# Performance work log

Hardware: AMD Instinct MI355X
Metric: run time of the kernel (lower is better)

The kernel has to match this reference:

```python
import jax, jax.numpy as jnp
import numpy as np

N_TOKENS = 16384
HIDDEN = 2048
N_EXPERTS = 256
N_GROUPS = 8
TOPK_GROUPS = 4
TOPK = 8
ROUTE_SCALE = 2.5


def setup_inputs() -> dict:
    key = jax.random.key(0)
    k1, k2, k3 = jax.random.split(key, 3)
    x = jax.random.normal(k1, (N_TOKENS, HIDDEN), dtype=jnp.float32)
    weight = jax.random.normal(k2, (N_EXPERTS, HIDDEN), dtype=jnp.float32) * 0.02
    bias = jax.random.normal(k3, (N_EXPERTS,), dtype=jnp.float32) * 0.02
    return {"x": x, "weight": weight, "bias": bias}


def reference(x, weight, bias):
    # linear scoring: [N, E]
    scores = jnp.einsum("nd,ed->ne", x, weight) + bias
    scores = jax.nn.sigmoid(scores)  # score_func == 'sigmoid'
    original_scores = scores
    # bias is not None -> add bias to routing scores
    scores = scores + bias
    n = x.shape[0]
    # grouped routing: [N, G, E/G]
    scores_g = scores.reshape(n, N_GROUPS, N_EXPERTS // N_GROUPS)
    # bias present -> group score = sum of top-2 per group
    top2_vals, _ = jax.lax.top_k(scores_g, 2)
    group_scores = top2_vals.sum(axis=-1)  # [N, G]
    _, grp_idx = jax.lax.top_k(group_scores, TOPK_GROUPS)  # [N, topk_groups]
    keep = jnp.zeros((n, N_GROUPS), dtype=bool).at[
        jnp.arange(n)[:, None], grp_idx
    ].set(True)
    masked = jnp.where(keep[:, :, None], scores_g, -jnp.inf).reshape(n, N_EXPERTS)
    # final top-k experts over masked scores
    _, indices = jax.lax.top_k(masked, TOPK)  # [N, topk]
    weights = jnp.take_along_axis(original_scores, indices, axis=1)
    # sigmoid -> normalize selected weights
    weights = weights / weights.sum(axis=-1, keepdims=True)
    weights = (weights * ROUTE_SCALE).astype(x.dtype)
    return weights, indices
```

## Files before the change

### kernel.cpp

```cpp
#include <hip/hip_runtime.h>
#include <math.h>

#define NT 16384
#define HID 2048
#define NE 256
#define NG 8
#define TOPG 4
#define TOPKK 8

constexpr int BM = 64;
constexpr int KC = 32;

__global__ __launch_bounds__(512) void score_kernel(
    const float* __restrict__ x, const float* __restrict__ w,
    const float* __restrict__ bias, double* __restrict__ sd)
{
    __shared__ float xs[KC][BM];
    __shared__ float wsm[KC][NE];

    const int tid = threadIdx.x;
    const int tx = tid & 31;
    const int ty = tid >> 5;
    const int m0 = blockIdx.x * BM;

    const int xrow = tid & 63;
    const int xko  = (tid >> 6) * 4;
    const int wexp = tid & 255;
    const int wko  = (tid >> 8) * 16;

    double accd[4][8];
#pragma unroll
    for (int mi = 0; mi < 4; mi++)
#pragma unroll
        for (int j = 0; j < 8; j++) accd[mi][j] = 0.0;

    const float* wbase = w + (size_t)wexp * HID + wko;
    const float* xbase = x + (size_t)(m0 + xrow) * HID + xko;

    for (int k0 = 0; k0 < HID; k0 += KC) {
        float4 wv0 = *(const float4*)(wbase + k0 + 0);
        float4 wv1 = *(const float4*)(wbase + k0 + 4);
        float4 wv2 = *(const float4*)(wbase + k0 + 8);
        float4 wv3 = *(const float4*)(wbase + k0 + 12);
        float4 xv  = *(const float4*)(xbase + k0);

        __syncthreads();

        wsm[wko +  0][wexp] = wv0.x; wsm[wko +  1][wexp] = wv0.y;
        wsm[wko +  2][wexp] = wv0.z; wsm[wko +  3][wexp] = wv0.w;
        wsm[wko +  4][wexp] = wv1.x; wsm[wko +  5][wexp] = wv1.y;
        wsm[wko +  6][wexp] = wv1.z; wsm[wko +  7][wexp] = wv1.w;
        wsm[wko +  8][wexp] = wv2.x; wsm[wko +  9][wexp] = wv2.y;
        wsm[wko + 10][wexp] = wv2.z; wsm[wko + 11][wexp] = wv2.w;
        wsm[wko + 12][wexp] = wv3.x; wsm[wko + 13][wexp] = wv3.y;
        wsm[wko + 14][wexp] = wv3.z; wsm[wko + 15][wexp] = wv3.w;
        xs[xko + 0][xrow] = xv.x;
        xs[xko + 1][xrow] = xv.y;
        xs[xko + 2][xrow] = xv.z;
        xs[xko + 3][xrow] = xv.w;

        __syncthreads();

        float accf[4][8];

        {
            float4 a  = *(const float4*)&xs[0][ty * 4];
            float4 b0 = *(const float4*)&wsm[0][tx * 4];
            float4 b1 = *(const float4*)&wsm[0][128 + tx * 4];
            float av[4] = {a.x, a.y, a.z, a.w};
            float bv[8] = {b0.x, b0.y, b0.z, b0.w, b1.x, b1.y, b1.z, b1.w};
#pragma unroll
            for (int mi = 0; mi < 4; mi++)
#pragma unroll
                for (int j = 0; j < 8; j++)
                    accf[mi][j] = av[mi] * bv[j];
        }

#pragma unroll
        for (int kk = 1; kk < KC; kk++) {
            float4 a  = *(const float4*)&xs[kk][ty * 4];
            float4 b0 = *(const float4*)&wsm[kk][tx * 4];
            float4 b1 = *(const float4*)&wsm[kk][128 + tx * 4];
            float av[4] = {a.x, a.y, a.z, a.w};
            float bv[8] = {b0.x, b0.y, b0.z, b0.w, b1.x, b1.y, b1.z, b1.w};
#pragma unroll
            for (int mi = 0; mi < 4; mi++)
#pragma unroll
                for (int j = 0; j < 8; j++)
                    accf[mi][j] = fmaf(av[mi], bv[j], accf[mi][j]);
        }

#pragma unroll
        for (int mi = 0; mi < 4; mi++)
#pragma unroll
            for (int j = 0; j < 8; j++) accd[mi][j] += (double)accf[mi][j];
    }

#pragma unroll
    for (int mi = 0; mi < 4; mi++) {
        const size_t row = (size_t)(m0 + ty * 4 + mi) * NE;
#pragma unroll
        for (int j = 0; j < 8; j++) {
            const int n = (j < 4) ? (tx * 4 + j) : (128 + tx * 4 + (j - 4));
            double z = accd[mi][j] + (double)bias[n];
            double s = 1.0 / (1.0 + exp(-z));
            sd[row + n] = s;
        }
    }
}

__global__ __launch_bounds__(256) void route_kernel(
    const double* __restrict__ sd, const float* __restrict__ bias,
    float* __restrict__ wout, float* __restrict__ iout)
{
    const int lane = threadIdx.x & 63;
    const int wid  = threadIdx.x >> 6;
    const int tok  = blockIdx.x * 4 + wid;
    const double* srow = sd + (size_t)tok * NE;
    const int e0 = lane * 4;

    const double NEG = -__builtin_inf();

    double s0 = srow[e0 + 0], s1 = srow[e0 + 1], s2 = srow[e0 + 2], s3 = srow[e0 + 3];
    double sb0 = s0 + (double)bias[e0 + 0];
    double sb1 = s1 + (double)bias[e0 + 1];
    double sb2 = s2 + (double)bias[e0 + 2];
    double sb3 = s3 + (double)bias[e0 + 3];

    double m1 = sb0, m2 = NEG;
    if (sb1 > m1) { m2 = m1; m1 = sb1; } else if (sb1 > m2) m2 = sb1;
    if (sb2 > m1) { m2 = m1; m1 = sb2; } else if (sb2 > m2) m2 = sb2;
    if (sb3 > m1) { m2 = m1; m1 = sb3; } else if (sb3 > m2) m2 = sb3;

#pragma unroll
    for (int mask = 1; mask <= 4; mask <<= 1) {
        double o1 = __shfl_xor(m1, mask);
        double o2 = __shfl_xor(m2, mask);
        double n1 = fmax(m1, o1);
        double n2 = fmax(fmin(m1, o1), fmax(m2, o2));
        m1 = n1; m2 = n2;
    }
    double gs = m1 + m2;

    double g[8];
#pragma unroll
    for (int j = 0; j < 8; j++) g[j] = __shfl(gs, j * 8);

    const int myg = lane >> 3;
    int rank = 0;
#pragma unroll
    for (int j = 0; j < 8; j++)
        rank += (g[j] > g[myg] || (g[j] == g[myg] && j < myg)) ? 1 : 0;
    const bool keep = (rank < TOPG);

    double v0 = keep ? sb0 : NEG;
    double v1 = keep ? sb1 : NEG;
    double v2 = keep ? sb2 : NEG;
    double v3 = keep ? sb3 : NEG;

    double wv[TOPKK];
    int    idx[TOPKK];

#pragma unroll
    for (int r = 0; r < TOPKK; r++) {
        double bvv = v0; int bi = e0;
        if (v1 > bvv) { bvv = v1; bi = e0 + 1; }
        if (v2 > bvv) { bvv = v2; bi = e0 + 2; }
        if (v3 > bvv) { bvv = v3; bi = e0 + 3; }
#pragma unroll
        for (int mask = 1; mask <= 32; mask <<= 1) {
            double ov = __shfl_xor(bvv, mask);
            int    oi = __shfl_xor(bi, mask);
            if (ov > bvv || (ov == bvv && oi < bi)) { bvv = ov; bi = oi; }
        }
        const int sel   = bi & 3;
        const int owner = bi >> 2;
        double cands = (sel == 0) ? s0 : (sel == 1) ? s1 : (sel == 2) ? s2 : s3;
        wv[r]  = __shfl(cands, owner);
        idx[r] = bi;
        if (lane == owner) {
            if (sel == 0) v0 = NEG;
            else if (sel == 1) v1 = NEG;
            else if (sel == 2) v2 = NEG;
            else v3 = NEG;
        }
    }

    double sum = 0.0;
#pragma unroll
    for (int r = 0; r < TOPKK; r++) sum += wv[r];
    const double scale = 2.5 / sum;

    if (lane == 0) {
#pragma unroll
        for (int r = 0; r < TOPKK; r++)
            wout[(size_t)tok * TOPKK + r] = (float)(wv[r] * scale);
#pragma unroll
        for (int r = 0; r < TOPKK; r++)
            iout[(size_t)tok * TOPKK + r] = (float)idx[r];
    }
}

extern "C" void kernel_launch(void* const* d_in, const int* in_sizes, int n_in,
                              void* d_out, int out_size, void* d_ws, size_t ws_size,
                              hipStream_t stream) {
    const float* x = (const float*)d_in[0];
    const float* w = (const float*)d_in[1];
    const float* b = (const float*)d_in[2];

    double* sd = (double*)d_ws;
    float* wout = (float*)d_out;
    float* iout = wout + (size_t)NT * TOPKK;

    score_kernel<<<NT / BM, 512, 0, stream>>>(x, w, b, sd);
    route_kernel<<<NT / 4, 256, 0, stream>>>(sd, b, wout, iout);
}
```

Before: 422.0 us.

## Halve score tile to 32 rows and prefetch next K-chunk into registers

Shrinks the score kernel block to 32 token rows with 256 threads, doubling the grid. Each thread now loads one full expert row chunk of 32 floats. The global loads for the next K chunk are issued after the shared-memory store, so they overlap the current chunk's compute. The costs are more register pressure from the 8 prefetched float4 and twice the weight traffic per token, since each block reuses the weight tile over fewer rows.

```diff
diff --git a/kernel.cpp b/kernel.cpp
--- a/kernel.cpp
+++ b/kernel.cpp
@@ -8,10 +8,10 @@
 #define TOPG 4
 #define TOPKK 8
 
-constexpr int BM = 64;
+constexpr int BM = 32;
 constexpr int KC = 32;
 
-__global__ __launch_bounds__(512) void score_kernel(
+__global__ __launch_bounds__(256) void score_kernel(
     const float* __restrict__ x, const float* __restrict__ w,
     const float* __restrict__ bias, double* __restrict__ sd)
 {
@@ -23,10 +23,11 @@
     const int ty = tid >> 5;
     const int m0 = blockIdx.x * BM;
 
-    const int xrow = tid & 63;
-    const int xko  = (tid >> 6) * 4;
-    const int wexp = tid & 255;
-    const int wko  = (tid >> 8) * 16;
+    const int xrow = tid & 31;
+    const int xko  = (tid >> 5) * 4;
+
+    const float* wbase = w + (size_t)tid * HID;
+    const float* xbase = x + (size_t)(m0 + xrow) * HID + xko;
 
     double accd[4][8];
 #pragma unroll
@@ -34,30 +35,33 @@
 #pragma unroll
         for (int j = 0; j < 8; j++) accd[mi][j] = 0.0;
 
-    const float* wbase = w + (size_t)wexp * HID + wko;
-    const float* xbase = x + (size_t)(m0 + xrow) * HID + xko;
+    float4 wr[8];
+    float4 xr;
+#pragma unroll
+    for (int q = 0; q < 8; q++) wr[q] = *(const float4*)(wbase + q * 4);
+    xr = *(const float4*)(xbase);
 
     for (int k0 = 0; k0 < HID; k0 += KC) {
-        float4 wv0 = *(const float4*)(wbase + k0 + 0);
-        float4 wv1 = *(const float4*)(wbase + k0 + 4);
-        float4 wv2 = *(const float4*)(wbase + k0 + 8);
-        float4 wv3 = *(const float4*)(wbase + k0 + 12);
-        float4 xv  = *(const float4*)(xbase + k0);
-
         __syncthreads();
 
-        wsm[wko +  0][wexp] = wv0.x; wsm[wko +  1][wexp] = wv0.y;
-        wsm[wko +  2][wexp] = wv0.z; wsm[wko +  3][wexp] = wv0.w;
-        wsm[wko +  4][wexp] = wv1.x; wsm[wko +  5][wexp] = wv1.y;
-        wsm[wko +  6][wexp] = wv1.z; wsm[wko +  7][wexp] = wv1.w;
-        wsm[wko +  8][wexp] = wv2.x; wsm[wko +  9][wexp] = wv2.y;
-        wsm[wko + 10][wexp] = wv2.z; wsm[wko + 11][wexp] = wv2.w;
-        wsm[wko + 12][wexp] = wv3.x; wsm[wko + 13][wexp] = wv3.y;
-        wsm[wko + 14][wexp] = wv3.z; wsm[wko + 15][wexp] = wv3.w;
-        xs[xko + 0][xrow] = xv.x;
-        xs[xko + 1][xrow] = xv.y;
-        xs[xko + 2][xrow] = xv.z;
-        xs[xko + 3][xrow] = xv.w;
+#pragma unroll
+        for (int q = 0; q < 8; q++) {
+            wsm[q * 4 + 0][tid] = wr[q].x;
+            wsm[q * 4 + 1][tid] = wr[q].y;
+            wsm[q * 4 + 2][tid] = wr[q].z;
+            wsm[q * 4 + 3][tid] = wr[q].w;
+        }
+        xs[xko + 0][xrow] = xr.x;
+        xs[xko + 1][xrow] = xr.y;
+        xs[xko + 2][xrow] = xr.z;
+        xs[xko + 3][xrow] = xr.w;
+
+        if (k0 + KC < HID) {
+#pragma unroll
+            for (int q = 0; q < 8; q++)
+                wr[q] = *(const float4*)(wbase + k0 + KC + q * 4);
+            xr = *(const float4*)(xbase + k0 + KC);
+        }
 
         __syncthreads();
 
@@ -212,6 +216,6 @@
     float* wout = (float*)d_out;
     float* iout = wout + (size_t)NT * TOPKK;
 
-    score_kernel<<<NT / BM, 512, 0, stream>>>(x, w, b, sd);
+    score_kernel<<<NT / BM, 256, 0, stream>>>(x, w, b, sd);
     route_kernel<<<NT / 4, 256, 0, stream>>>(sd, b, wout, iout);
 }
```

New measurement: 438.1 us. +3.8%, slower.
